# Performance work log

Hardware: AMD Instinct MI355X
Metric: run time of the kernel (lower is better)

Reference implementation:

```python
import jax, jax.numpy as jnp
import numpy as np

B, N, F_IN, F_OUT = 8, 2048, 128, 128


def setup_inputs() -> dict:
    key = jax.random.key(0)
    k1, k2, k3, k4 = jax.random.split(key, 4)
    h = jax.random.normal(k1, (B, N, F_IN), dtype=jnp.float32)
    adj = (jax.random.uniform(k2, (B, N, N)) > 0.5).astype(jnp.float32)
    adj = jnp.maximum(adj, jnp.eye(N, dtype=jnp.float32)[None])
    # torch nn.Linear weights: W is [out_features, in_features], a is [1, 2*out_features]
    W = jax.random.normal(k3, (F_OUT, F_IN), dtype=jnp.float32) * 0.05
    a = jax.random.normal(k4, (1, 2 * F_OUT), dtype=jnp.float32) * 0.05
    return {"h": h, "adj": adj, "W": W, "a": a}


def reference(h, adj, W, a):
    # Wh = W(h): [B, N, F_OUT]
    Wh = jnp.einsum("bnf,of->bno", h, W)
    # attn_fc(concat(Wh_i, Wh_j)) == (Wh_i @ a1) + (Wh_j @ a2): exact split of the
    # linear layer, avoiding the O(B*N*N*2F) concat intermediate.
    a1 = a[0, :F_OUT]
    a2 = a[0, F_OUT:]
    e_i = Wh @ a1  # [B, N]  score contribution of destination node i
    e_j = Wh @ a2  # [B, N]  score contribution of source node j
    e = e_i[:, :, None] + e_j[:, None, :]  # [B, N, N]
    e = e + (1.0 - adj) * (-1e9)
    alpha = jax.nn.softmax(e, axis=-1)  # [B, N, N]
    # weighted aggregation: h_out[b,i] = sum_j alpha[b,i,j] * Wh[b,j]
    h_out = jnp.einsum("bij,bjo->bio", alpha, Wh)
    return h_out
```

## Files before the change

### kernel.cpp

```cpp
#include <hip/hip_runtime.h>
#include <stdint.h>

#define AS1 __attribute__((address_space(1)))
#define AS3 __attribute__((address_space(3)))

typedef __bf16 bf16x8 __attribute__((ext_vector_type(8)));
typedef float f32x4 __attribute__((ext_vector_type(4)));

constexpr int NB = 8;
constexpr int N  = 2048;
constexpr int F  = 128;

__device__ __forceinline__ unsigned short bf16r(float f) {
    unsigned u = __float_as_uint(f);
    return (unsigned short)((u + 0x7FFFu + ((u >> 16) & 1u)) >> 16);
}
__device__ __forceinline__ float bf2f(unsigned short s) {
    return __uint_as_float(((unsigned)s) << 16);
}


__global__ __launch_bounds__(256) void k1_wh(const float* __restrict__ h,
                                             const float* __restrict__ W,
                                             const float* __restrict__ a,
                                             unsigned short* __restrict__ Wb2,
                                             unsigned short* __restrict__ p16) {
    __shared__ float epart[2][64];

    const int tid  = threadIdx.x;
    const int lane = tid & 63, wid = tid >> 6;
    const int quad = lane >> 4, l15 = lane & 15;
    const int wm = wid >> 1, wn = wid & 1;
    const int m0 = blockIdx.x * 64;
    const int batch = m0 >> 11;
    const int nbase = m0 & 2047;

    f32x4 acc[2][4] = {};

#pragma unroll
    for (int kk = 0; kk < 4; ++kk) {
        const int k = kk * 32 + quad * 8;
        bf16x8 afr[2], bfr[4];
#pragma unroll
        for (int rt = 0; rt < 2; ++rt) {
            const float* src = h + (size_t)(m0 + wm * 32 + rt * 16 + l15) * F + k;
            float4 x0 = *(const float4*)src;
            float4 x1 = *(const float4*)(src + 4);
            afr[rt][0] = (__bf16)x0.x; afr[rt][1] = (__bf16)x0.y;
            afr[rt][2] = (__bf16)x0.z; afr[rt][3] = (__bf16)x0.w;
            afr[rt][4] = (__bf16)x1.x; afr[rt][5] = (__bf16)x1.y;
            afr[rt][6] = (__bf16)x1.z; afr[rt][7] = (__bf16)x1.w;
        }
#pragma unroll
        for (int ct = 0; ct < 4; ++ct) {
            const int o = wn * 64 + ct * 16 + l15;
            const float* src = W + (size_t)o * F + k;
            float4 x0 = *(const float4*)src;
            float4 x1 = *(const float4*)(src + 4);
            bfr[ct][0] = (__bf16)x0.x; bfr[ct][1] = (__bf16)x0.y;
            bfr[ct][2] = (__bf16)x0.z; bfr[ct][3] = (__bf16)x0.w;
            bfr[ct][4] = (__bf16)x1.x; bfr[ct][5] = (__bf16)x1.y;
            bfr[ct][6] = (__bf16)x1.z; bfr[ct][7] = (__bf16)x1.w;
        }
#pragma unroll
        for (int rt = 0; rt < 2; ++rt)
#pragma unroll
            for (int ct = 0; ct < 4; ++ct)
                acc[rt][ct] = __builtin_amdgcn_mfma_f32_16x16x32_bf16(
                    afr[rt], bfr[ct], acc[rt][ct], 0, 0, 0);
    }

    float a2v[4];
#pragma unroll
    for (int ct = 0; ct < 4; ++ct) a2v[ct] = a[F + wn * 64 + ct * 16 + l15];

    float ep[2][4];
#pragma unroll
    for (int rt = 0; rt < 2; ++rt)
#pragma unroll
        for (int g = 0; g < 4; ++g) {
            float s = 0.f;
#pragma unroll
            for (int ct = 0; ct < 4; ++ct) s += acc[rt][ct][g] * a2v[ct];
            ep[rt][g] = s;
        }
#pragma unroll
    for (int m = 1; m < 16; m <<= 1)
#pragma unroll
        for (int rt = 0; rt < 2; ++rt)
#pragma unroll
            for (int g = 0; g < 4; ++g)
                ep[rt][g] += __shfl_xor(ep[rt][g], m);

    if (l15 == 0)
#pragma unroll
        for (int rt = 0; rt < 2; ++rt)
#pragma unroll
            for (int g = 0; g < 4; ++g)
                epart[wn][wm * 32 + rt * 16 + quad * 4 + g] = ep[rt][g];
    __syncthreads();

#pragma unroll
    for (int rt = 0; rt < 2; ++rt)
#pragma unroll
        for (int ct = 0; ct < 4; ++ct) {
            const int o  = wn * 64 + ct * 16 + l15;
            const int r0 = wm * 32 + rt * 16 + quad * 4;
            const int n0 = nbase + r0;
            ushort4 v;
#pragma unroll
            for (int g = 0; g < 4; ++g) {
                const float e  = epart[0][r0 + g] + epart[1][r0 + g];
                const float pf = bf2f(bf16r(expf(e)));
                (&v.x)[g] = bf16r(pf * acc[rt][ct][g]);
            }
            size_t off = (size_t)batch * N * F + (size_t)(n0 >> 3) * 1024 + o * 8 + (n0 & 7);
            *(ushort4*)&Wb2[off] = v;
        }

    if (tid < 64) {
        const float e = epart[0][tid] + epart[1][tid];
        p16[batch * N + nbase + tid] = bf16r(expf(e));
    }
}

__global__ __launch_bounds__(256) void k3_attn(const float* __restrict__ adj,
                                               const unsigned short* __restrict__ Wb2,
                                               const unsigned short* __restrict__ p16,
                                               float* __restrict__ out) {
    __shared__ __align__(16) float At[2][32 * 64];

    const int tid  = threadIdx.x;
    const int lane = tid & 63, wid = tid >> 6;
    const int quad = lane >> 4, l15 = lane & 15;
    const int wm = wid >> 1, wn = wid & 1;
    const int b  = blockIdx.x & 7;
    const int i0 = (blockIdx.x >> 3) * 32;

    const float* adjb = adj + (size_t)b * N * N;
    const char*  bB   = (const char*)Wb2 + (size_t)b * N * F * 2 + wn * 1024 + l15 * 16;
    const unsigned short* pb = p16 + b * N;

    const int lrow = lane >> 4, lslot = lane & 15;
    auto stage = [&](int buf, int c) {
#pragma unroll
        for (int s = 0; s < 2; ++s) {
            const int ii = wid * 2 + s;
            const int ri = ii * 4 + lrow;
            const int gf = ((lslot ^ (ri & 15)) << 2);
            const float* g = adjb + (size_t)(i0 + ri) * N + c * 64 + gf;
            __builtin_amdgcn_global_load_lds((const AS1 void*)g,
                (AS3 void*)((char*)&At[buf][0] + ii * 1024), 16, 0, 0);
        }
    };

    f32x4 acc[4] = {};
    f32x4 dacc = {};

    stage(0, 0);

    for (int c = 0; c < 32; ++c) {
        const int cur = c & 1;
        __syncthreads();
        if (c + 1 < 32) stage(cur ^ 1, c + 1);

#pragma unroll
        for (int ks = 0; ks < 2; ++ks) {
            const char* rowb = (const char*)&At[cur][0] + (wm * 16 + l15) * 256;
            const int slot0 = (ks * 8 + quad * 2) ^ l15;
            f32x4 x0 = *(const f32x4*)(rowb + slot0 * 16);
            f32x4 x1 = *(const f32x4*)(rowb + (slot0 ^ 1) * 16);

            const char* bp = bB + ((size_t)c * 8 + ks * 4 + quad) * 2048;
            bf16x8 b0 = *(const bf16x8*)bp;
            bf16x8 b1 = *(const bf16x8*)(bp + 256);
            bf16x8 b2 = *(const bf16x8*)(bp + 512);
            bf16x8 b3 = *(const bf16x8*)(bp + 768);
            bf16x8 pv = *(const bf16x8*)(pb + c * 64 + ks * 32 + quad * 8);

            bf16x8 af;
            af[0] = (__bf16)x0[0]; af[1] = (__bf16)x0[1];
            af[2] = (__bf16)x0[2]; af[3] = (__bf16)x0[3];
            af[4] = (__bf16)x1[0]; af[5] = (__bf16)x1[1];
            af[6] = (__bf16)x1[2]; af[7] = (__bf16)x1[3];

            acc[0] = __builtin_amdgcn_mfma_f32_16x16x32_bf16(af, b0, acc[0], 0, 0, 0);
            acc[1] = __builtin_amdgcn_mfma_f32_16x16x32_bf16(af, b1, acc[1], 0, 0, 0);
            acc[2] = __builtin_amdgcn_mfma_f32_16x16x32_bf16(af, b2, acc[2], 0, 0, 0);
            acc[3] = __builtin_amdgcn_mfma_f32_16x16x32_bf16(af, b3, acc[3], 0, 0, 0);
            dacc   = __builtin_amdgcn_mfma_f32_16x16x32_bf16(af, pv, dacc, 0, 0, 0);
        }
    }

    float inv[4];
#pragma unroll
    for (int g = 0; g < 4; ++g) inv[g] = 1.0f / dacc[g];

    float* ob = out + (size_t)b * N * F;
#pragma unroll
    for (int ct = 0; ct < 4; ++ct) {
        const int o = wn * 64 + ct * 16 + l15;
#pragma unroll
        for (int g = 0; g < 4; ++g) {
            const int i = i0 + wm * 16 + quad * 4 + g;
            ob[(size_t)i * F + o] = acc[ct][g] * inv[g];
        }
    }
}

extern "C" void kernel_launch(void* const* d_in, const int* in_sizes, int n_in,
                              void* d_out, int out_size, void* d_ws, size_t ws_size,
                              hipStream_t stream) {
    const float* h   = (const float*)d_in[0];
    const float* adj = (const float*)d_in[1];
    const float* W   = (const float*)d_in[2];
    const float* a   = (const float*)d_in[3];
    float* out = (float*)d_out;

    unsigned short* Wb2 = (unsigned short*)d_ws;
    unsigned short* p16 = (unsigned short*)((char*)d_ws + (4u << 20));

    k1_wh<<<NB * N / 64, 256, 0, stream>>>(h, W, a, Wb2, p16);
    k3_attn<<<NB * (N / 32), 256, 0, stream>>>(adj, Wb2, p16, out);
}
```

Measured before the change: 228.8 us.

## Retile attention kernel to 16-row blocks with triple-buffered inline-asm LDS pipeline

Each attention block now covers 16 destination rows instead of 32, doubling the grid, and each wave owns 32 output columns. The adjacency tile is staged into a three-deep LDS ring using inline-asm global_load_lds issued two chunks ahead. Wh and p loads are issued as explicit asm, with manual vmcnt waits and raw s_barrier. The goal is more parallelism and overlap of the dominant adjacency stream with MFMA work. In exchange, each Wh/p chunk is read by twice as many blocks, and the hand-written waitcnt/barrier synchronisation is fragile.

```diff
diff --git a/kernel.cpp b/kernel.cpp
--- a/kernel.cpp
+++ b/kernel.cpp
@@ -128,69 +128,93 @@
                                                const unsigned short* __restrict__ Wb2,
                                                const unsigned short* __restrict__ p16,
                                                float* __restrict__ out) {
-    __shared__ __align__(16) float At[2][32 * 64];
+    __shared__ __align__(16) float At[3][16 * 64];
 
     const int tid  = threadIdx.x;
     const int lane = tid & 63, wid = tid >> 6;
     const int quad = lane >> 4, l15 = lane & 15;
-    const int wm = wid >> 1, wn = wid & 1;
     const int b  = blockIdx.x & 7;
-    const int i0 = (blockIdx.x >> 3) * 32;
-
-    const float* adjb = adj + (size_t)b * N * N;
-    const char*  bB   = (const char*)Wb2 + (size_t)b * N * F * 2 + wn * 1024 + l15 * 16;
-    const unsigned short* pb = p16 + b * N;
-
-    const int lrow = lane >> 4, lslot = lane & 15;
-    auto stage = [&](int buf, int c) {
-#pragma unroll
-        for (int s = 0; s < 2; ++s) {
-            const int ii = wid * 2 + s;
-            const int ri = ii * 4 + lrow;
-            const int gf = ((lslot ^ (ri & 15)) << 2);
-            const float* g = adjb + (size_t)(i0 + ri) * N + c * 64 + gf;
-            __builtin_amdgcn_global_load_lds((const AS1 void*)g,
-                (AS3 void*)((char*)&At[buf][0] + ii * 1024), 16, 0, 0);
-        }
-    };
-
-    f32x4 acc[4] = {};
+    const int i0 = (blockIdx.x >> 3) * 16;
+
+    const int ri = wid * 4 + (lane >> 4);
+    const int lslot = lane & 15;
+    const char* aSt = (const char*)adj
+        + ((size_t)b * N * N + (size_t)(i0 + ri) * N + ((lslot ^ ri) << 2)) * 4;
+    unsigned lds0 = (unsigned)(size_t)(AS3 char*)((char*)&At[0][0] + wid * 1024);
+    lds0 = __builtin_amdgcn_readfirstlane(lds0);
+    const unsigned ldsA[3] = { lds0, lds0 + 4096u, lds0 + 8192u };
+
+    const char* WbB = (const char*)Wb2 + (size_t)b * N * F * 2
+                    + wid * 512 + l15 * 16;
+    const char* pB  = (const char*)p16 + (size_t)b * N * 2 + quad * 16;
+
+    f32x4 acc[2] = {};
     f32x4 dacc = {};
 
-    stage(0, 0);
-
-    for (int c = 0; c < 32; ++c) {
-        const int cur = c & 1;
-        __syncthreads();
-        if (c + 1 < 32) stage(cur ^ 1, c + 1);
-
-#pragma unroll
-        for (int ks = 0; ks < 2; ++ks) {
-            const char* rowb = (const char*)&At[cur][0] + (wm * 16 + l15) * 256;
-            const int slot0 = (ks * 8 + quad * 2) ^ l15;
-            f32x4 x0 = *(const f32x4*)(rowb + slot0 * 16);
-            f32x4 x1 = *(const f32x4*)(rowb + (slot0 ^ 1) * 16);
-
-            const char* bp = bB + ((size_t)c * 8 + ks * 4 + quad) * 2048;
-            bf16x8 b0 = *(const bf16x8*)bp;
-            bf16x8 b1 = *(const bf16x8*)(bp + 256);
-            bf16x8 b2 = *(const bf16x8*)(bp + 512);
-            bf16x8 b3 = *(const bf16x8*)(bp + 768);
-            bf16x8 pv = *(const bf16x8*)(pb + c * 64 + ks * 32 + quad * 8);
-
-            bf16x8 af;
-            af[0] = (__bf16)x0[0]; af[1] = (__bf16)x0[1];
-            af[2] = (__bf16)x0[2]; af[3] = (__bf16)x0[3];
-            af[4] = (__bf16)x1[0]; af[5] = (__bf16)x1[1];
-            af[6] = (__bf16)x1[2]; af[7] = (__bf16)x1[3];
-
-            acc[0] = __builtin_amdgcn_mfma_f32_16x16x32_bf16(af, b0, acc[0], 0, 0, 0);
-            acc[1] = __builtin_amdgcn_mfma_f32_16x16x32_bf16(af, b1, acc[1], 0, 0, 0);
-            acc[2] = __builtin_amdgcn_mfma_f32_16x16x32_bf16(af, b2, acc[2], 0, 0, 0);
-            acc[3] = __builtin_amdgcn_mfma_f32_16x16x32_bf16(af, b3, acc[3], 0, 0, 0);
-            dacc   = __builtin_amdgcn_mfma_f32_16x16x32_bf16(af, pv, dacc, 0, 0, 0);
-        }
-    }
+#define STAGE(C, WS)                                                          \
+    asm volatile("s_mov_b32 m0, %0\n\t"                                       \
+                 "global_load_lds_dwordx4 %1, off"                            \
+                 :: "s"(ldsA[WS]), "v"((uint64_t)(aSt + (size_t)(C) * 256))   \
+                 : "memory")
+
+#define BODY(C, RS, WS, DO_STAGE, VMSTR) do {                                 \
+    asm volatile("s_barrier" ::: "memory");                                   \
+    f32x4 b00, b01, b10, b11, p0, p1;                                         \
+    {                                                                         \
+        const char* bp0 = WbB + ((size_t)(C) * 8 + quad) * 2048;              \
+        const char* bp1 = bp0 + 4 * 2048;                                     \
+        asm volatile(                                                         \
+            "global_load_dwordx4 %0, %6, off\n\t"                             \
+            "global_load_dwordx4 %1, %7, off\n\t"                             \
+            "global_load_dwordx4 %2, %8, off\n\t"                             \
+            "global_load_dwordx4 %3, %9, off\n\t"                             \
+            "global_load_dwordx4 %4, %10, off\n\t"                            \
+            "global_load_dwordx4 %5, %11, off"                                \
+            : "=&v"(b00), "=&v"(b01), "=&v"(b10), "=&v"(b11),                 \
+              "=&v"(p0), "=&v"(p1)                                            \
+            : "v"((uint64_t)bp0), "v"((uint64_t)(bp0 + 256)),                 \
+              "v"((uint64_t)bp1), "v"((uint64_t)(bp1 + 256)),                 \
+              "v"((uint64_t)(pB + (size_t)(C) * 128)),                        \
+              "v"((uint64_t)(pB + (size_t)(C) * 128 + 64))                    \
+            : "memory");                                                      \
+    }                                                                         \
+    if (DO_STAGE) STAGE((C) + 2, WS);                                         \
+    asm volatile("s_waitcnt " VMSTR                                           \
+        : "+v"(b00), "+v"(b01), "+v"(b10), "+v"(b11), "+v"(p0), "+v"(p1)      \
+        :: "memory");                                                         \
+    const char* rowb = (const char*)&At[RS][0] + l15 * 256;                   \
+    _Pragma("unroll")                                                         \
+    for (int ks = 0; ks < 2; ++ks) {                                          \
+        const int g0 = ks * 8 + quad * 2;                                     \
+        f32x4 x0 = *(const f32x4*)(rowb + ((g0 ^ l15) << 4));                 \
+        f32x4 x1 = *(const f32x4*)(rowb + (((g0 + 1) ^ l15) << 4));           \
+        bf16x8 af;                                                            \
+        af[0] = (__bf16)x0[0]; af[1] = (__bf16)x0[1];                         \
+        af[2] = (__bf16)x0[2]; af[3] = (__bf16)x0[3];                         \
+        af[4] = (__bf16)x1[0]; af[5] = (__bf16)x1[1];                         \
+        af[6] = (__bf16)x1[2]; af[7] = (__bf16)x1[3];                         \
+        acc[0] = __builtin_amdgcn_mfma_f32_16x16x32_bf16(                     \
+            af, __builtin_bit_cast(bf16x8, ks ? b10 : b00), acc[0], 0, 0, 0); \
+        acc[1] = __builtin_amdgcn_mfma_f32_16x16x32_bf16(                     \
+            af, __builtin_bit_cast(bf16x8, ks ? b11 : b01), acc[1], 0, 0, 0); \
+        dacc   = __builtin_amdgcn_mfma_f32_16x16x32_bf16(                     \
+            af, __builtin_bit_cast(bf16x8, ks ? p1 : p0), dacc, 0, 0, 0);     \
+    }                                                                         \
+} while (0)
+
+    STAGE(0, 0);
+    STAGE(1, 1);
+
+    for (int c = 0; c < 30; c += 3) {
+        BODY(c + 0, 0, 2, 1, "vmcnt(1)");
+        BODY(c + 1, 1, 0, 1, "vmcnt(1)");
+        BODY(c + 2, 2, 1, 1, "vmcnt(1)");
+    }
+    BODY(30, 0, 0, 0, "vmcnt(0)");
+    BODY(31, 1, 0, 0, "vmcnt(0)");
+
+#undef STAGE
+#undef BODY
 
     float inv[4];
 #pragma unroll
@@ -198,11 +222,11 @@
 
     float* ob = out + (size_t)b * N * F;
 #pragma unroll
-    for (int ct = 0; ct < 4; ++ct) {
-        const int o = wn * 64 + ct * 16 + l15;
+    for (int ct = 0; ct < 2; ++ct) {
+        const int o = wid * 32 + ct * 16 + l15;
 #pragma unroll
         for (int g = 0; g < 4; ++g) {
-            const int i = i0 + wm * 16 + quad * 4 + g;
+            const int i = i0 + quad * 4 + g;
             ob[(size_t)i * F + o] = acc[ct][g] * inv[g];
         }
     }
@@ -221,5 +245,5 @@
     unsigned short* p16 = (unsigned short*)((char*)d_ws + (4u << 20));
 
     k1_wh<<<NB * N / 64, 256, 0, stream>>>(h, W, a, Wb2, p16);
-    k3_attn<<<NB * (N / 32), 256, 0, stream>>>(adj, Wb2, p16, out);
-}
+    k3_attn<<<NB * (N / 16), 256, 0, stream>>>(adj, Wb2, p16, out);
+}
```

Result: slower. 238.3 us (+4.2%).

## Stage Wh tiles in LDS and shrink attention row tile to 16

Applied to the files above, without the earlier changes.

The attention kernel now uses 16-row output tiles and splits the 128 output columns across four waves, instead of a 2x2 wave grid over 32 rows. Besides the adjacency tile, each block also stages the bf16 Wh chunk into double-buffered LDS with async global-to-LDS loads, so waves no longer read it straight from global memory. This doubles the grid, which should help occupancy and latency hiding for the adj stream. The cost is that every block reloads the full Wh column panel for half as many rows, doubling total Wh traffic, and uses more LDS per block.

```diff
diff --git a/kernel.cpp b/kernel.cpp
--- a/kernel.cpp
+++ b/kernel.cpp
@@ -128,33 +128,34 @@
                                                const unsigned short* __restrict__ Wb2,
                                                const unsigned short* __restrict__ p16,
                                                float* __restrict__ out) {
-    __shared__ __align__(16) float At[2][32 * 64];
+    __shared__ __align__(16) float          At[2][16 * 64];
+    __shared__ __align__(16) unsigned short Bt[2][8 * 1024];
 
     const int tid  = threadIdx.x;
     const int lane = tid & 63, wid = tid >> 6;
     const int quad = lane >> 4, l15 = lane & 15;
-    const int wm = wid >> 1, wn = wid & 1;
     const int b  = blockIdx.x & 7;
-    const int i0 = (blockIdx.x >> 3) * 32;
-
-    const float* adjb = adj + (size_t)b * N * N;
-    const char*  bB   = (const char*)Wb2 + (size_t)b * N * F * 2 + wn * 1024 + l15 * 16;
+    const int i0 = (blockIdx.x >> 3) * 16;
+
+    const int ri = wid * 4 + (lane >> 4);
+    const int lslot = lane & 15;
+    const float* aSrc = adj + (size_t)b * N * N + (size_t)(i0 + ri) * N
+                      + ((lslot ^ ri) << 2);
+    const char* bSrc = (const char*)Wb2 + (size_t)b * N * F * 2
+                     + (size_t)wid * 4096 + lane * 16;
     const unsigned short* pb = p16 + b * N;
 
-    const int lrow = lane >> 4, lslot = lane & 15;
     auto stage = [&](int buf, int c) {
-#pragma unroll
-        for (int s = 0; s < 2; ++s) {
-            const int ii = wid * 2 + s;
-            const int ri = ii * 4 + lrow;
-            const int gf = ((lslot ^ (ri & 15)) << 2);
-            const float* g = adjb + (size_t)(i0 + ri) * N + c * 64 + gf;
-            __builtin_amdgcn_global_load_lds((const AS1 void*)g,
-                (AS3 void*)((char*)&At[buf][0] + ii * 1024), 16, 0, 0);
-        }
+        __builtin_amdgcn_global_load_lds((const AS1 void*)(aSrc + c * 64),
+            (AS3 void*)((char*)&At[buf][0] + wid * 1024), 16, 0, 0);
+#pragma unroll
+        for (int s = 0; s < 4; ++s)
+            __builtin_amdgcn_global_load_lds(
+                (const AS1 void*)(bSrc + (size_t)c * 16384 + s * 1024),
+                (AS3 void*)((char*)&Bt[buf][0] + wid * 4096 + s * 1024), 16, 0, 0);
     };
 
-    f32x4 acc[4] = {};
+    f32x4 acc[2] = {};
     f32x4 dacc = {};
 
     stage(0, 0);
@@ -166,16 +167,14 @@
 
 #pragma unroll
         for (int ks = 0; ks < 2; ++ks) {
-            const char* rowb = (const char*)&At[cur][0] + (wm * 16 + l15) * 256;
-            const int slot0 = (ks * 8 + quad * 2) ^ l15;
-            f32x4 x0 = *(const f32x4*)(rowb + slot0 * 16);
-            f32x4 x1 = *(const f32x4*)(rowb + (slot0 ^ 1) * 16);
-
-            const char* bp = bB + ((size_t)c * 8 + ks * 4 + quad) * 2048;
-            bf16x8 b0 = *(const bf16x8*)bp;
-            bf16x8 b1 = *(const bf16x8*)(bp + 256);
-            bf16x8 b2 = *(const bf16x8*)(bp + 512);
-            bf16x8 b3 = *(const bf16x8*)(bp + 768);
+            const char* rowb = (const char*)&At[cur][0] + l15 * 256;
+            const int g0 = ks * 8 + quad * 2;
+            f32x4 x0 = *(const f32x4*)(rowb + ((g0 ^ l15) << 4));
+            f32x4 x1 = *(const f32x4*)(rowb + (((g0 + 1) ^ l15) << 4));
+            const char* bb = (const char*)&Bt[cur][0]
+                           + (ks * 4 + quad) * 2048 + wid * 512 + l15 * 16;
+            bf16x8 b0 = *(const bf16x8*)bb;
+            bf16x8 b1 = *(const bf16x8*)(bb + 256);
             bf16x8 pv = *(const bf16x8*)(pb + c * 64 + ks * 32 + quad * 8);
 
             bf16x8 af;
@@ -186,8 +185,6 @@
 
             acc[0] = __builtin_amdgcn_mfma_f32_16x16x32_bf16(af, b0, acc[0], 0, 0, 0);
             acc[1] = __builtin_amdgcn_mfma_f32_16x16x32_bf16(af, b1, acc[1], 0, 0, 0);
-            acc[2] = __builtin_amdgcn_mfma_f32_16x16x32_bf16(af, b2, acc[2], 0, 0, 0);
-            acc[3] = __builtin_amdgcn_mfma_f32_16x16x32_bf16(af, b3, acc[3], 0, 0, 0);
             dacc   = __builtin_amdgcn_mfma_f32_16x16x32_bf16(af, pv, dacc, 0, 0, 0);
         }
     }
@@ -198,11 +195,11 @@
 
     float* ob = out + (size_t)b * N * F;
 #pragma unroll
-    for (int ct = 0; ct < 4; ++ct) {
-        const int o = wn * 64 + ct * 16 + l15;
+    for (int ct = 0; ct < 2; ++ct) {
+        const int o = wid * 32 + ct * 16 + l15;
 #pragma unroll
         for (int g = 0; g < 4; ++g) {
-            const int i = i0 + wm * 16 + quad * 4 + g;
+            const int i = i0 + quad * 4 + g;
             ob[(size_t)i * F + o] = acc[ct][g] * inv[g];
         }
     }
@@ -221,5 +218,5 @@
     unsigned short* p16 = (unsigned short*)((char*)d_ws + (4u << 20));
 
     k1_wh<<<NB * N / 64, 256, 0, stream>>>(h, W, a, Wb2, p16);
-    k3_attn<<<NB * (N / 32), 256, 0, stream>>>(adj, Wb2, p16, out);
-}
+    k3_attn<<<NB * (N / 16), 256, 0, stream>>>(adj, Wb2, p16, out);
+}
```

New measurement: 220.3 us. 3.7% less time.
